# Performance work log

Measured on AMD Instinct MI355X. Metric: run time of the kernel, lower is better.

Reference implementation:

```python
import jax, jax.numpy as jnp
import numpy as np

NX, NY = 512, 512
DX, DY = 1e-4, 1e-4
VS = 1550.0
DT = 2.5e-8


def setup_inputs() -> dict:
    key = jax.random.key(0)
    k1, k2 = jax.random.split(key)
    sensor_data = jax.random.normal(k1, (4, 2, 128, 2048), dtype=jnp.float32)
    sensor_xy = jax.random.randint(k2, (128, 2), 0, 512, dtype=jnp.int32)
    return {"sensor_data": sensor_data, "sensor_xy": sensor_xy}


def _delay_indices(sensor_xy):
    # pixel grids, 1-indexed as in the torch code (arange(1,513))
    ix = jnp.arange(1, NX + 1, dtype=jnp.float32)[None, :, None]  # (1,Nx,1)
    iy = jnp.arange(1, NY + 1, dtype=jnp.float32)[None, None, :]  # (1,1,Ny)
    x = sensor_xy[:, 0].astype(jnp.float32)[:, None, None]        # (S,1,1)
    y = sensor_xy[:, 1].astype(jnp.float32)[:, None, None]
    dis = jnp.sqrt(((x - ix + 1.0) * DX) ** 2 + ((y - iy + 1.0) * DY) ** 2)  # (S,Nx,Ny)
    # .to(torch.long) truncates; values are non-negative so int cast matches
    return (dis / VS / DT).astype(jnp.int32).reshape(sensor_xy.shape[0], -1)  # (S, Nx*Ny)


def reference(sensor_data, sensor_xy):
    B = sensor_data.shape[0]
    S = sensor_xy.shape[0]
    t = _delay_indices(sensor_xy)                           # (S, P) int32
    data = jnp.transpose(sensor_data, (2, 0, 1, 3))         # (S, B, 2, T)

    def step(img, xs):
        t_s, d_s = xs                                       # (P,), (B,2,T)
        return img + d_s[:, :, t_s], None                   # gather + accumulate

    img0 = jnp.zeros((B, 2, NX * NY), dtype=sensor_data.dtype)
    img, _ = jax.lax.scan(step, img0, (t, data))
    return img.reshape(B, 2, NX, NY)
```

## Files before the change

kernel.cpp:

```cpp
#include <hip/hip_runtime.h>
#include <math.h>


#define NXY 512
#define S_CNT 128
#define T_CNT 2048
#define CH 8
#define CH_STRIDE (S_CNT * T_CNT)
#define NPIX (NXY * NXY)
#define TAB_BYTES (NPIX * 2)
#define CHUNK 8
#define NCHUNK (S_CNT / CHUNK)
#define WIN 64
#define PATW 24
#define PAT_ROW_B (PATW * 2)
#define PAT_SENS_B (16 * PAT_ROW_B)

typedef float f32x2 __attribute__((ext_vector_type(2)));

#if __has_builtin(__builtin_amdgcn_sad_u32)
__device__ __forceinline__ unsigned int sadu(unsigned int a, unsigned int b, unsigned int c) {
    return __builtin_amdgcn_sad_u32(a, b, c);
}
#else
__device__ __forceinline__ unsigned int sadu(unsigned int a, unsigned int b, unsigned int c) {
    return (a > b ? a - b : b - a) + c;
}
#endif

__device__ __forceinline__ unsigned short delay_entry(int adx, int ady) {
    const double DX32 = (double)1e-4f;
    const double R1 = (double)(float)(1.0 / 1550.0);
    const double R2 = (double)(float)(1.0 / (double)2.5e-8f);
    float dxf = (float)((double)adx * DX32);
    float dyf = (float)((double)ady * DX32);
    float a2 = (float)((double)dxf * (double)dxf);
    float b2 = (float)((double)dyf * (double)dyf);
    float sum = (float)((double)a2 + (double)b2);
    float dis = (float)sqrt((double)sum);
    float q1 = (float)((double)dis * R1);
    float q2 = (float)((double)q1 * R2);
    return (unsigned short)(int)q2;
}

__device__ __forceinline__ unsigned int bf16_rne(float f) {
    unsigned int x = __float_as_uint(f);
    return (x + 0x7fffu + ((x >> 16) & 1u)) >> 16;
}

__global__ __launch_bounds__(256) void prep(const float* __restrict__ data,
                                            unsigned short* __restrict__ tab,
                                            uint4* __restrict__ d2b) {
    int idx = blockIdx.x * 256 + threadIdx.x;
    tab[idx] = (unsigned short)((unsigned int)delay_entry(idx >> 9, idx & 511) << 4);

    unsigned int w[4];
#pragma unroll
    for (int j = 0; j < 4; ++j) {
        unsigned int lo = bf16_rne(data[(2 * j) * CH_STRIDE + idx]);
        unsigned int hi = bf16_rne(data[(2 * j + 1) * CH_STRIDE + idx]);
        w[j] = lo | (hi << 16);
    }
    d2b[idx] = make_uint4(w[0], w[1], w[2], w[3]);
}

__device__ __forceinline__ float bflo(unsigned int u) { return __uint_as_float(u << 16); }
__device__ __forceinline__ float bfhi(unsigned int u) { return __uint_as_float(u & 0xffff0000u); }

__device__ __forceinline__ unsigned int swz16(unsigned int d) {
    return d ^ (((d >> 7) & 3u) << 4);
}
__device__ __forceinline__ unsigned int subswz_x2(unsigned int a, unsigned int tm4) {
    unsigned int lo = swz16((a - tm4) & 0xffffu);
    unsigned int hi = swz16(((a >> 16) - tm4) & 0xffffu);
    return lo | (hi << 16);
}

__global__ __launch_bounds__(256) void das_win(const uint4* __restrict__ d2b,
                                               const unsigned short* __restrict__ tab,
                                               const int* __restrict__ sxy,
                                               float* __restrict__ out) {
    __shared__ uint4 minfo[S_CNT];
    __shared__ uint2 mstage[S_CNT];
    __shared__ uint4 winb[CHUNK * WIN];
    __shared__ uint4 patb[CHUNK * 16 * 3];

    int tid = threadIdx.x;
    int x0 = (blockIdx.x >> 5) << 4;
    int y0 = (blockIdx.x & 31) << 4;

    if (tid < S_CNT) {
        int sxv = sxy[2 * tid];
        int syv = sxy[2 * tid + 1];
        int axm = sxv < x0 ? x0 - sxv : (sxv > x0 + 15 ? sxv - x0 - 15 : 0);
        int aym = syv < y0 ? y0 - syv : (syv > y0 + 15 ? syv - y0 - 15 : 0);
        int ay0 = aym & ~7;
        int tmin = (int)delay_entry(axm, aym);
        minfo[tid] = make_uint4((unsigned int)sxv, (unsigned int)(2 * syv),
                                (unsigned int)(-(axm * 48 + ay0 * 2)), 0u);
        mstage[tid] = make_uint2((unsigned int)(axm | (ay0 << 16)),
                                 (unsigned int)(tmin << 4));
    }
    __syncthreads();

    int iy = y0 | (((tid >> 6) & 1) << 3) | (tid & 7);
    int ix = x0 | ((tid >> 7) << 3) | ((tid >> 3) & 7);
    unsigned int uix = (unsigned int)ix;
    unsigned int uiy2 = (unsigned int)(2 * iy);

    f32x2 acc2[4];
#pragma unroll
    for (int k = 0; k < 4; ++k) acc2[k] = (f32x2){0.0f, 0.0f};

    char* winc = (char*)winb;
    char* patc = (char*)patb;

    for (int c = 0; c < NCHUNK; ++c) {
        int s0 = c * CHUNK;

        {
            int lsw = tid >> 5;
            int e0 = tid & 31;
            uint2 st = mstage[s0 + lsw];
            const uint4* src = d2b + ((size_t)(s0 + lsw) << 11) + (st.y >> 4) + e0;
            unsigned int sw = (((unsigned int)e0 >> 3) & 3u) << 4;
            unsigned int slot = ((unsigned int)lsw << 10) | (((unsigned int)e0 << 4) ^ sw);
            uint4 v0 = src[0];
            uint4 v1 = src[32];
            *(uint4*)(winc + slot) = v0;
            *(uint4*)(winc + slot + 512u) = v1;
        }

#pragma unroll
        for (int j = 0; j < 2; ++j) {
            unsigned int idx = (unsigned int)tid + 256u * j;
            if (idx < 384u) {
                unsigned int r3 = idx / 3u;
                unsigned int cc = idx - r3 * 3u;
                unsigned int row = r3 & 15u;
                unsigned int ls = r3 >> 4;
                uint2 st = mstage[s0 + ls];
                int ax0 = (int)(st.x & 0xffffu);
                int ay0 = (int)(st.x >> 16);
                unsigned int tm4 = st.y;
                uint4 v = *(const uint4*)((const char*)tab +
                    (((size_t)(ax0 + (int)row) << 10) + ((size_t)ay0 << 1) + ((size_t)cc << 4)));
                v.x = subswz_x2(v.x, tm4);
                v.y = subswz_x2(v.y, tm4);
                v.z = subswz_x2(v.z, tm4);
                v.w = subswz_x2(v.w, tm4);
                patb[ls * 48u + row * 3u + cc] = v;
            }
        }
        __syncthreads();

        unsigned int t16[CHUNK];
#pragma unroll
        for (int j = 0; j < CHUNK; ++j) {
            uint4 mi = minfo[s0 + j];
            unsigned int b1 = sadu(mi.x, uix, 0u);
            unsigned int b2 = sadu(mi.y, uiy2, mi.z);
            unsigned int byte = b1 * 48u + b2;
            t16[j] = (unsigned int)*(const unsigned short*)(
                patc + (unsigned int)(j * PAT_SENS_B) + byte);
        }

#pragma unroll
        for (int j = 0; j < CHUNK; ++j) {
            uint4 w = *(const uint4*)(winc + (unsigned int)(j << 10) + t16[j]);
            f32x2 p0 = {bflo(w.x), bfhi(w.x)};
            f32x2 p1 = {bflo(w.y), bfhi(w.y)};
            f32x2 p2 = {bflo(w.z), bfhi(w.z)};
            f32x2 p3 = {bflo(w.w), bfhi(w.w)};
            acc2[0] += p0;
            acc2[1] += p1;
            acc2[2] += p2;
            acc2[3] += p3;
        }
        __syncthreads();
    }

    int pix = (ix << 9) | iy;
#pragma unroll
    for (int k = 0; k < 4; ++k) {
        out[(2 * k) * NPIX + pix] = acc2[k].x;
        out[(2 * k + 1) * NPIX + pix] = acc2[k].y;
    }
}

__global__ __launch_bounds__(256) void build_table(unsigned short* __restrict__ tab) {
    int idx = blockIdx.x * 256 + threadIdx.x;
    tab[idx] = delay_entry(idx >> 9, idx & 511);
}

__global__ __launch_bounds__(256) void das_main(const float* __restrict__ data,
                                                const unsigned short* __restrict__ tab,
                                                const int* __restrict__ sxy,
                                                float* __restrict__ out) {
    __shared__ int sx[S_CNT];
    __shared__ int sy[S_CNT];
    int tid = threadIdx.x;
    if (tid < S_CNT) {
        sx[tid] = sxy[2 * tid];
        sy[tid] = sxy[2 * tid + 1];
    }
    __syncthreads();
    int iy = ((blockIdx.x & 31) << 4) | (tid & 15);
    int ix = ((blockIdx.x >> 5) << 4) | (tid >> 4);
    float acc[CH];
#pragma unroll
    for (int k = 0; k < CH; ++k) acc[k] = 0.0f;
#pragma unroll 4
    for (int s = 0; s < S_CNT; ++s) {
        int dxi = sx[s] - ix;
        int dyi = sy[s] - iy;
        int adx = dxi < 0 ? -dxi : dxi;
        int ady = dyi < 0 ? -dyi : dyi;
        int t = (int)tab[(adx << 9) | ady];
        const float* p = data + (s << 11) + t;
#pragma unroll
        for (int k = 0; k < CH; ++k) acc[k] += p[(size_t)k * CH_STRIDE];
    }
    int pix = (ix << 9) | iy;
#pragma unroll
    for (int k = 0; k < CH; ++k) out[k * NPIX + pix] = acc[k];
}

extern "C" void kernel_launch(void* const* d_in, const int* in_sizes, int n_in,
                              void* d_out, int out_size, void* d_ws, size_t ws_size,
                              hipStream_t stream) {
    const float* data = (const float*)d_in[0];
    const int* sxy = (const int*)d_in[1];
    float* out = (float*)d_out;
    unsigned short* tab = (unsigned short*)d_ws;

    size_t need = (size_t)TAB_BYTES + (size_t)CH_STRIDE * 16;
    if (ws_size >= need) {
        uint4* d2b = (uint4*)((char*)d_ws + TAB_BYTES);
        prep<<<NPIX / 256, 256, 0, stream>>>(data, tab, d2b);
        das_win<<<1024, 256, 0, stream>>>(d2b, tab, sxy, out);
    } else {
        build_table<<<NPIX / 256, 256, 0, stream>>>(tab);
        das_main<<<1024, 256, 0, stream>>>(data, tab, sxy, out);
    }
}
```

Before: 101.5 us.

## Double-buffer window/pattern staging and precompute per-tile sensor metadata in prep

The main kernel now double-buffers its shared-memory window and delay-pattern tiles, issuing the global loads for the next sensor chunk before computing the current one and writing them to shared memory afterwards, so one barrier per chunk remains and load latency can overlap compute. Per-tile, per-sensor metadata (bounding offsets and minimum delay) moves into the prep kernel and is stored in workspace, and the main kernel reads it straight from global memory inside the gather loop. This costs twice the shared memory (lower occupancy), more live registers, and an extra 2 MB workspace buffer. The delay table is located by negative pointer arithmetic from the d2b pointer.

```diff
diff --git a/kernel.cpp b/kernel.cpp
--- a/kernel.cpp
+++ b/kernel.cpp
@@ -8,13 +8,15 @@
 #define CH 8
 #define CH_STRIDE (S_CNT * T_CNT)
 #define NPIX (NXY * NXY)
+#define NTILE 1024
 #define TAB_BYTES (NPIX * 2)
+#define D2B_BYTES (CH_STRIDE * 16)
+#define META_BYTES (NTILE * S_CNT * 16)
 #define CHUNK 8
 #define NCHUNK (S_CNT / CHUNK)
 #define WIN 64
 #define PATW 24
-#define PAT_ROW_B (PATW * 2)
-#define PAT_SENS_B (16 * PAT_ROW_B)
+#define PAT_SENS_B (16 * PATW * 2)
 
 typedef float f32x2 __attribute__((ext_vector_type(2)));
 
@@ -49,8 +51,10 @@
 }
 
 __global__ __launch_bounds__(256) void prep(const float* __restrict__ data,
+                                            const int* __restrict__ sxy,
                                             unsigned short* __restrict__ tab,
-                                            uint4* __restrict__ d2b) {
+                                            uint4* __restrict__ d2b,
+                                            uint4* __restrict__ meta) {
     int idx = blockIdx.x * 256 + threadIdx.x;
     tab[idx] = (unsigned short)((unsigned int)delay_entry(idx >> 9, idx & 511) << 4);
 
@@ -62,6 +66,22 @@
         w[j] = lo | (hi << 16);
     }
     d2b[idx] = make_uint4(w[0], w[1], w[2], w[3]);
+
+    if (idx < NTILE * S_CNT) {
+        int tile = idx >> 7;
+        int s = idx & 127;
+        int x0 = (tile >> 5) << 4;
+        int y0 = (tile & 31) << 4;
+        int sxv = sxy[2 * s];
+        int syv = sxy[2 * s + 1];
+        int axm = sxv < x0 ? x0 - sxv : (sxv > x0 + 15 ? sxv - x0 - 15 : 0);
+        int aym = syv < y0 ? y0 - syv : (syv > y0 + 15 ? syv - y0 - 15 : 0);
+        int ay0 = aym & ~7;
+        int tmin = (int)delay_entry(axm, aym);
+        meta[idx] = make_uint4((unsigned int)sxv, (unsigned int)(2 * syv),
+                               (unsigned int)(axm | (ay0 << 16)),
+                               (unsigned int)(tmin << 4));
+    }
 }
 
 __device__ __forceinline__ float bflo(unsigned int u) { return __uint_as_float(u << 16); }
@@ -76,33 +96,24 @@
     return lo | (hi << 16);
 }
 
-__global__ __launch_bounds__(256) void das_win(const uint4* __restrict__ d2b,
-                                               const unsigned short* __restrict__ tab,
-                                               const int* __restrict__ sxy,
-                                               float* __restrict__ out) {
-    __shared__ uint4 minfo[S_CNT];
+__global__ __launch_bounds__(256) void das_smeta(const uint4* __restrict__ d2b,
+                                                 const uint4* __restrict__ meta,
+                                                 float* __restrict__ out) {
     __shared__ uint2 mstage[S_CNT];
-    __shared__ uint4 winb[CHUNK * WIN];
-    __shared__ uint4 patb[CHUNK * 16 * 3];
+    __shared__ uint4 winb[2][CHUNK * WIN];
+    __shared__ uint4 patb[2][CHUNK * 16 * 3];
 
     int tid = threadIdx.x;
+    const uint4* mblk = meta + ((size_t)blockIdx.x << 7);
+
+    if (tid < S_CNT) {
+        uint4 m = mblk[tid];
+        mstage[tid] = make_uint2(m.z, m.w);
+    }
+    __syncthreads();
+
+    int y0 = (blockIdx.x & 31) << 4;
     int x0 = (blockIdx.x >> 5) << 4;
-    int y0 = (blockIdx.x & 31) << 4;
-
-    if (tid < S_CNT) {
-        int sxv = sxy[2 * tid];
-        int syv = sxy[2 * tid + 1];
-        int axm = sxv < x0 ? x0 - sxv : (sxv > x0 + 15 ? sxv - x0 - 15 : 0);
-        int aym = syv < y0 ? y0 - syv : (syv > y0 + 15 ? syv - y0 - 15 : 0);
-        int ay0 = aym & ~7;
-        int tmin = (int)delay_entry(axm, aym);
-        minfo[tid] = make_uint4((unsigned int)sxv, (unsigned int)(2 * syv),
-                                (unsigned int)(-(axm * 48 + ay0 * 2)), 0u);
-        mstage[tid] = make_uint2((unsigned int)(axm | (ay0 << 16)),
-                                 (unsigned int)(tmin << 4));
-    }
-    __syncthreads();
-
     int iy = y0 | (((tid >> 6) & 1) << 3) | (tid & 7);
     int ix = x0 | ((tid >> 7) << 3) | ((tid >> 3) & 7);
     unsigned int uix = (unsigned int)ix;
@@ -112,73 +123,108 @@
 #pragma unroll
     for (int k = 0; k < 4; ++k) acc2[k] = (f32x2){0.0f, 0.0f};
 
-    char* winc = (char*)winb;
-    char* patc = (char*)patb;
+    uint4 rw0, rw1;
+    uint4 rp0, rp1;
+    unsigned int wslot, pslot0, pslot1, ptm0, ptm1;
+    const int lsw = tid >> 5, e0 = tid & 31;
+    const unsigned int swn = (((unsigned int)e0 >> 3) & 3u) << 4;
+    const bool p1act = tid < 128;
+
+#define ISSUE(cc)                                                                     \
+    {                                                                                 \
+        int s0n = (cc) * CHUNK;                                                       \
+        uint2 stw = mstage[s0n + lsw];                                                \
+        const uint4* wsrc = d2b + ((size_t)(s0n + lsw) << 11) + (stw.y >> 4) + e0;    \
+        rw0 = wsrc[0];                                                                \
+        rw1 = wsrc[32];                                                               \
+        wslot = ((unsigned int)lsw << 10) | (((unsigned int)e0 << 4) ^ swn);          \
+        {                                                                             \
+            unsigned int pidx = (unsigned int)tid;                                    \
+            unsigned int r3 = pidx / 3u, cc2 = pidx - r3 * 3u;                        \
+            unsigned int row = r3 & 15u, ls = r3 >> 4;                                \
+            uint2 stp = mstage[s0n + ls];                                             \
+            rp0 = *(const uint4*)((const char*)tab_g +                                \
+                ((((stp.x & 0xffffu) + row) << 10) + ((stp.x >> 16) << 1) + (cc2 << 4))); \
+            pslot0 = ls * 768u + row * 48u + cc2 * 16u;                               \
+            ptm0 = stp.y;                                                             \
+        }                                                                             \
+        if (p1act) {                                                                  \
+            unsigned int pidx = (unsigned int)tid + 256u;                             \
+            unsigned int r3 = pidx / 3u, cc2 = pidx - r3 * 3u;                        \
+            unsigned int row = r3 & 15u, ls = r3 >> 4;                                \
+            uint2 stp = mstage[s0n + ls];                                             \
+            rp1 = *(const uint4*)((const char*)tab_g +                                \
+                ((((stp.x & 0xffffu) + row) << 10) + ((stp.x >> 16) << 1) + (cc2 << 4))); \
+            pslot1 = ls * 768u + row * 48u + cc2 * 16u;                               \
+            ptm1 = stp.y;                                                             \
+        }                                                                             \
+    }
+
+#define WRITEBUF(cc)                                                                  \
+    {                                                                                 \
+        char* wb = (char*)winb[(cc) & 1];                                             \
+        char* pb = (char*)patb[(cc) & 1];                                             \
+        *(uint4*)(wb + wslot) = rw0;                                                  \
+        *(uint4*)(wb + wslot + 512u) = rw1;                                           \
+        uint4 v = rp0;                                                                \
+        v.x = subswz_x2(v.x, ptm0);                                                   \
+        v.y = subswz_x2(v.y, ptm0);                                                   \
+        v.z = subswz_x2(v.z, ptm0);                                                   \
+        v.w = subswz_x2(v.w, ptm0);                                                   \
+        *(uint4*)(pb + pslot0) = v;                                                   \
+        if (p1act) {                                                                  \
+            uint4 u = rp1;                                                            \
+            u.x = subswz_x2(u.x, ptm1);                                               \
+            u.y = subswz_x2(u.y, ptm1);                                               \
+            u.z = subswz_x2(u.z, ptm1);                                               \
+            u.w = subswz_x2(u.w, ptm1);                                               \
+            *(uint4*)(pb + pslot1) = u;                                               \
+        }                                                                             \
+    }
+
+    const char* tab_g = (const char*)d2b - TAB_BYTES;
+
+    ISSUE(0);
+    WRITEBUF(0);
+    __syncthreads();
 
     for (int c = 0; c < NCHUNK; ++c) {
-        int s0 = c * CHUNK;
+        if (c + 1 < NCHUNK) ISSUE(c + 1);
 
         {
-            int lsw = tid >> 5;
-            int e0 = tid & 31;
-            uint2 st = mstage[s0 + lsw];
-            const uint4* src = d2b + ((size_t)(s0 + lsw) << 11) + (st.y >> 4) + e0;
-            unsigned int sw = (((unsigned int)e0 >> 3) & 3u) << 4;
-            unsigned int slot = ((unsigned int)lsw << 10) | (((unsigned int)e0 << 4) ^ sw);
-            uint4 v0 = src[0];
-            uint4 v1 = src[32];
-            *(uint4*)(winc + slot) = v0;
-            *(uint4*)(winc + slot + 512u) = v1;
-        }
-
-#pragma unroll
-        for (int j = 0; j < 2; ++j) {
-            unsigned int idx = (unsigned int)tid + 256u * j;
-            if (idx < 384u) {
-                unsigned int r3 = idx / 3u;
-                unsigned int cc = idx - r3 * 3u;
-                unsigned int row = r3 & 15u;
-                unsigned int ls = r3 >> 4;
-                uint2 st = mstage[s0 + ls];
-                int ax0 = (int)(st.x & 0xffffu);
-                int ay0 = (int)(st.x >> 16);
-                unsigned int tm4 = st.y;
-                uint4 v = *(const uint4*)((const char*)tab +
-                    (((size_t)(ax0 + (int)row) << 10) + ((size_t)ay0 << 1) + ((size_t)cc << 4)));
-                v.x = subswz_x2(v.x, tm4);
-                v.y = subswz_x2(v.y, tm4);
-                v.z = subswz_x2(v.z, tm4);
-                v.w = subswz_x2(v.w, tm4);
-                patb[ls * 48u + row * 3u + cc] = v;
+            const char* patc = (const char*)patb[c & 1];
+            const char* winc = (const char*)winb[c & 1];
+            int s0 = c * CHUNK;
+            unsigned int t16[CHUNK];
+#pragma unroll
+            for (int j = 0; j < CHUNK; ++j) {
+                uint4 m = mblk[s0 + j];
+                unsigned int Cc = 0u - ((m.z & 0xffffu) * 48u + (m.z >> 16) * 2u);
+                unsigned int b1 = sadu(m.x, uix, 0u);
+                unsigned int b2 = sadu(m.y, uiy2, 0u);
+                unsigned int byte = b1 * 48u + b2 + Cc;
+                t16[j] = (unsigned int)*(const unsigned short*)(
+                    patc + (unsigned int)(j * PAT_SENS_B) + byte);
+            }
+#pragma unroll
+            for (int j = 0; j < CHUNK; ++j) {
+                uint4 w = *(const uint4*)(winc + (unsigned int)(j << 10) + t16[j]);
+                f32x2 p0 = {bflo(w.x), bfhi(w.x)};
+                f32x2 p1 = {bflo(w.y), bfhi(w.y)};
+                f32x2 p2 = {bflo(w.z), bfhi(w.z)};
+                f32x2 p3 = {bflo(w.w), bfhi(w.w)};
+                acc2[0] += p0;
+                acc2[1] += p1;
+                acc2[2] += p2;
+                acc2[3] += p3;
             }
         }
+
+        if (c + 1 < NCHUNK) WRITEBUF(c + 1);
         __syncthreads();
-
-        unsigned int t16[CHUNK];
-#pragma unroll
-        for (int j = 0; j < CHUNK; ++j) {
-            uint4 mi = minfo[s0 + j];
-            unsigned int b1 = sadu(mi.x, uix, 0u);
-            unsigned int b2 = sadu(mi.y, uiy2, mi.z);
-            unsigned int byte = b1 * 48u + b2;
-            t16[j] = (unsigned int)*(const unsigned short*)(
-                patc + (unsigned int)(j * PAT_SENS_B) + byte);
-        }
-
-#pragma unroll
-        for (int j = 0; j < CHUNK; ++j) {
-            uint4 w = *(const uint4*)(winc + (unsigned int)(j << 10) + t16[j]);
-            f32x2 p0 = {bflo(w.x), bfhi(w.x)};
-            f32x2 p1 = {bflo(w.y), bfhi(w.y)};
-            f32x2 p2 = {bflo(w.z), bfhi(w.z)};
-            f32x2 p3 = {bflo(w.w), bfhi(w.w)};
-            acc2[0] += p0;
-            acc2[1] += p1;
-            acc2[2] += p2;
-            acc2[3] += p3;
-        }
-        __syncthreads();
-    }
+    }
+#undef ISSUE
+#undef WRITEBUF
 
     int pix = (ix << 9) | iy;
 #pragma unroll
@@ -234,11 +280,12 @@
     float* out = (float*)d_out;
     unsigned short* tab = (unsigned short*)d_ws;
 
-    size_t need = (size_t)TAB_BYTES + (size_t)CH_STRIDE * 16;
+    size_t need = (size_t)TAB_BYTES + (size_t)D2B_BYTES + (size_t)META_BYTES;
     if (ws_size >= need) {
         uint4* d2b = (uint4*)((char*)d_ws + TAB_BYTES);
-        prep<<<NPIX / 256, 256, 0, stream>>>(data, tab, d2b);
-        das_win<<<1024, 256, 0, stream>>>(d2b, tab, sxy, out);
+        uint4* meta = (uint4*)((char*)d_ws + TAB_BYTES + D2B_BYTES);
+        prep<<<NPIX / 256, 256, 0, stream>>>(data, sxy, tab, d2b, meta);
+        das_smeta<<<NTILE, 256, 0, stream>>>(d2b, meta, out);
     } else {
         build_table<<<NPIX / 256, 256, 0, stream>>>(tab);
         das_main<<<1024, 256, 0, stream>>>(data, tab, sxy, out);
```

After: 100.8 us. Within noise of the previous version (-0.7%).
